# Performance work log

Measured on AMD Instinct MI355X. Metric: run time of the kernel, lower is better.

The kernel has to match this reference:

```python
import jax, jax.numpy as jnp
import numpy as np

TOP_K = 2


def setup_inputs() -> dict:
    key = jax.random.key(0)
    k1, k2, k3, k4 = jax.random.split(key, 4)
    B, S, H, I, E = 8, 2048, 768, 3072, 8
    x = jax.random.normal(k1, (B, S, H), dtype=jnp.float32)
    # kaiming_uniform-ish scale for weights
    router_w = jax.random.uniform(k2, (E, H), dtype=jnp.float32, minval=-1.0, maxval=1.0) * (1.0 / np.sqrt(H))
    up_w = jax.random.uniform(k3, (E, H, I), dtype=jnp.float32, minval=-1.0, maxval=1.0) * (1.0 / np.sqrt(H))
    down_w = jax.random.uniform(k4, (E, I, H), dtype=jnp.float32, minval=-1.0, maxval=1.0) * (1.0 / np.sqrt(I))
    return {"x": x, "router_w": router_w, "up_w": up_w, "down_w": down_w}


def reference(x, router_w, up_w, down_w):
    B, S, H = x.shape
    E = up_w.shape[0]
    T = B * S
    xf = x.reshape(T, H)
    # router: Linear(H -> E, bias=False) then softmax, top-k, renormalize
    logits = xf @ router_w.T                      # [T, E]
    probs = jax.nn.softmax(logits, axis=-1)
    top_w, top_i = jax.lax.top_k(probs, TOP_K)    # [T, K]
    top_w = top_w / jnp.sum(top_w, axis=-1, keepdims=True)
    # dense per-(token, expert) gate: zero for unselected experts
    gate = jnp.zeros((T, E), dtype=xf.dtype).at[jnp.arange(T)[:, None], top_i].add(top_w)
    # combine: sum_e gate[:, e] * down_e(gelu(up_e(x)))
    out = jnp.zeros_like(xf)
    for e in range(E):  # fixed small expert count; loop is structural, not over data dims
        h = jax.nn.gelu(xf @ up_w[e], approximate=False)   # exact GELU == torch F.gelu
        out = out + gate[:, e:e + 1] * (h @ down_w[e])
    return out.reshape(B, S, H)
```

## Files before the change

kernel.cpp:

```cpp
#include <hip/hip_runtime.h>

typedef short bf16x8 __attribute__((ext_vector_type(8)));
typedef float f32x4  __attribute__((ext_vector_type(4)));

#define T_TOK 16384
#define HD 768
#define ID 3072
#define NE 8
#define NT1MAX 136

__device__ __forceinline__ unsigned short f2bf(float f) {
    unsigned int u = __float_as_uint(f);
    unsigned int r = (u + 0x7FFFu + ((u >> 16) & 1u)) >> 16;
    return (unsigned short)r;
}

__device__ __forceinline__ void gload16(const void* g, void* l) {
    __builtin_amdgcn_global_load_lds(
        (const __attribute__((address_space(1))) void*)g,
        (__attribute__((address_space(3))) void*)l, 16, 0, 0);
}

__device__ __forceinline__ float gelu_f(float x) {
    float z = fabsf(x) * 0.70710678118f;
    float t = 1.0f / fmaf(0.3275911f, z, 1.0f);
    float p = t * fmaf(t, fmaf(t, fmaf(t, fmaf(t, 1.061405429f, -1.453152027f),
                                       1.421413741f), -0.284496736f), 0.254829592f);
    float e = 1.0f - p * __expf(-z * z);
    float erfv = (x >= 0.f) ? e : -e;
    return 0.5f * x * (1.0f + erfv);
}

__device__ __forceinline__ int xcd_swz(int bid, int nwg) {
    int q = nwg >> 3, rr = nwg & 7;
    int xcd = bid & 7, seq = bid >> 3;
    return (xcd < rr ? xcd * (q + 1) : rr * (q + 1) + (xcd - rr) * q) + seq;
}

__global__ __launch_bounds__(256) void k_tp(const float* __restrict__ in,
                                            unsigned short* __restrict__ out,
                                            int R, int C) {
    __shared__ float t[64][65];
    const float* ine = in + (size_t)blockIdx.z * R * C;
    unsigned short* oute = out + (size_t)blockIdx.z * R * C;
    int c0 = blockIdx.x * 64, r0 = blockIdx.y * 64;
    int lc = threadIdx.x & 63, lr4 = threadIdx.x >> 6;
#pragma unroll
    for (int i = 0; i < 16; i++) {
        int r = i * 4 + lr4;
        t[r][lc] = ine[(size_t)(r0 + r) * C + c0 + lc];
    }
    __syncthreads();
#pragma unroll
    for (int i = 0; i < 16; i++) {
        int r = i * 4 + lr4;
        oute[(size_t)(c0 + r) * R + r0 + lc] = f2bf(t[lc][r]);
    }
}

__global__ __launch_bounds__(256) void k_router(const float* __restrict__ x,
                                                const float* __restrict__ rw,
                                                unsigned short* __restrict__ xb,
                                                int* __restrict__ topE,
                                                float* __restrict__ topW) {
    __shared__ float lrw[NE * HD];
    for (int i = threadIdx.x; i < NE * HD; i += 256) lrw[i] = rw[i];
    {
        const float4* xs4 = (const float4*)(x + (size_t)blockIdx.x * 4 * HD);
        ushort4* xb4 = (ushort4*)(xb + (size_t)blockIdx.x * 4 * HD);
#pragma unroll
        for (int i = 0; i < 3; i++) {
            float4 v = xs4[threadIdx.x + i * 256];
            ushort4 o;
            o.x = f2bf(v.x); o.y = f2bf(v.y); o.z = f2bf(v.z); o.w = f2bf(v.w);
            xb4[threadIdx.x + i * 256] = o;
        }
    }
    __syncthreads();
    int lane = threadIdx.x & 63;
    int t = blockIdx.x * 4 + (threadIdx.x >> 6);
    const float* xr = x + (size_t)t * HD;
    float acc[NE] = {0, 0, 0, 0, 0, 0, 0, 0};
    for (int h = lane; h < HD; h += 64) {
        float xv = xr[h];
#pragma unroll
        for (int e = 0; e < NE; e++) acc[e] = fmaf(xv, lrw[e * HD + h], acc[e]);
    }
#pragma unroll
    for (int e = 0; e < NE; e++) {
        float v = acc[e];
#pragma unroll
        for (int o = 32; o > 0; o >>= 1) v += __shfl_xor(v, o, 64);
        acc[e] = v;
    }
    if (lane == 0) {
        int e1 = 0; float l1 = acc[0];
#pragma unroll
        for (int e = 1; e < NE; e++) if (acc[e] > l1) { l1 = acc[e]; e1 = e; }
        int e2 = -1; float l2 = -1e30f;
#pragma unroll
        for (int e = 0; e < NE; e++) if (e != e1 && acc[e] > l2) { l2 = acc[e]; e2 = e; }
        float ex = expf(l2 - l1);
        float w1 = 1.0f / (1.0f + ex);
        topE[2 * t] = e1; topE[2 * t + 1] = e2;
        topW[2 * t] = w1; topW[2 * t + 1] = ex * w1;
    }
}

__global__ __launch_bounds__(256) void k_scatter(const int* __restrict__ topE,
                                                 const float* __restrict__ topW,
                                                 int* __restrict__ counts,
                                                 int* __restrict__ tokL,
                                                 float* __restrict__ gateL) {
    __shared__ int lc[NE], lbase[NE];
    if (threadIdx.x < NE) lc[threadIdx.x] = 0;
    __syncthreads();
    int t = blockIdx.x * 256 + threadIdx.x;
    int e1 = topE[2 * t], e2 = topE[2 * t + 1];
    int p1 = atomicAdd(&lc[e1], 1);
    int p2 = atomicAdd(&lc[e2], 1);
    __syncthreads();
    if (threadIdx.x < NE) lbase[threadIdx.x] = atomicAdd(&counts[threadIdx.x], lc[threadIdx.x]);
    __syncthreads();
    int q1 = lbase[e1] + p1, q2 = lbase[e2] + p2;
    tokL[e1 * T_TOK + q1] = t;  gateL[e1 * T_TOK + q1] = topW[2 * t];
    tokL[e2 * T_TOK + q2] = t;  gateL[e2 * T_TOK + q2] = topW[2 * t + 1];
}

__global__ void k_desc(const int* __restrict__ counts, int* __restrict__ tileE,
                       int* __restrict__ tileM0) {
    if (threadIdx.x == 0 && blockIdx.x == 0) {
        int tl = 0;
        for (int e = 0; e < NE; e++) {
            int c = counts[e];
            int nt = (c + 255) >> 8;
            for (int t = 0; t < nt; t++) { tileE[tl] = e; tileM0[tl] = t << 8; tl++; }
        }
        for (; tl < NT1MAX; tl++) { tileE[tl] = -1; tileM0[tl] = 0; }
    }
}

__global__ __launch_bounds__(512, 1) void k_gemm1(
    const unsigned short* __restrict__ xb,
    const unsigned short* __restrict__ upt,
    const int* __restrict__ tokL,
    const int* __restrict__ counts,
    const int* __restrict__ tileE,
    const int* __restrict__ tileM0,
    unsigned short* __restrict__ h,
    int seg, int ntn, int ldh) {
    __shared__ __align__(16) char lds[5][32768];
    constexpr int NK = HD / 32;
    int L = xcd_swz(blockIdx.x, gridDim.x);
    int mt = L / ntn, ntl = L - mt * ntn;
    int e = tileE[mt];
    if (e < 0) return;
    int m0 = tileM0[mt];
    int nrow = min(256, counts[e] - m0);
    const int* tok = tokL + e * T_TOK + m0;
    int n0 = (seg * ntn + ntl) * 256;

    const int tid = threadIdx.x, lane = tid & 63, wid = tid >> 6;
    const int wm = wid >> 2, wn = wid & 3;
    const int g = lane >> 4, r = lane & 15;

    int ar0 = wid * 16 + r;
    int ar1 = 128 + wid * 16 + r;
    const char* a0 = (const char*)(xb + (size_t)tok[ar0 < nrow ? ar0 : 0] * HD) + g * 16;
    const char* a1 = (const char*)(xb + (size_t)tok[ar1 < nrow ? ar1 : 0] * HD) + g * 16;
    const char* bsl = (const char*)(upt + (size_t)e * ID * HD);
    const char* b0 = bsl + (size_t)(n0 + wid * 16 + r) * (HD * 2) + g * 16;
    const char* b1 = bsl + (size_t)(n0 + 128 + wid * 16 + r) * (HD * 2) + g * 16;
    const int dst = wid * 1024;

    auto issue = [&](int step, int slot) {
        char* base = &lds[slot][0];
        int kb = step * 64;
        gload16(a0 + kb, base + dst);
        gload16(a1 + kb, base + 8192 + dst);
        gload16(b0 + kb, base + 16384 + dst);
        gload16(b1 + kb, base + 24576 + dst);
    };

    f32x4 acc[8][4];
#pragma unroll
    for (int m = 0; m < 8; m++)
#pragma unroll
        for (int n = 0; n < 4; n++) acc[m][n] = (f32x4){0.f, 0.f, 0.f, 0.f};

    issue(0, 0); issue(1, 1); issue(2, 2); issue(3, 3);
    asm volatile("s_waitcnt vmcnt(12)" ::: "memory");
    __builtin_amdgcn_s_barrier();
    asm volatile("" ::: "memory");

    const int aoff = wm * 8192 + g * 256 + r * 16;
    const int boff = 16384 + wn * 4096 + g * 256 + r * 16;

    for (int k = 0; k < NK; k++) {
        char* base = &lds[k % 5][0];
        bf16x8 a[4], b[4];
#pragma unroll
        for (int n = 0; n < 4; n++) b[n] = *(const bf16x8*)(base + boff + n * 1024);
#pragma unroll
        for (int m = 0; m < 4; m++) a[m] = *(const bf16x8*)(base + aoff + m * 1024);
        issue(min(k + 4, NK - 1), (k + 4) % 5);
        __builtin_amdgcn_s_setprio(1);
#pragma unroll
        for (int m = 0; m < 4; m++)
#pragma unroll
            for (int n = 0; n < 4; n++)
                acc[m][n] = __builtin_amdgcn_mfma_f32_16x16x32_bf16(a[m], b[n], acc[m][n], 0, 0, 0);
        __builtin_amdgcn_s_setprio(0);
#pragma unroll
        for (int m = 0; m < 4; m++) a[m] = *(const bf16x8*)(base + aoff + (4 + m) * 1024);
        __builtin_amdgcn_s_setprio(1);
#pragma unroll
        for (int m = 0; m < 4; m++)
#pragma unroll
            for (int n = 0; n < 4; n++)
                acc[4 + m][n] = __builtin_amdgcn_mfma_f32_16x16x32_bf16(a[m], b[n], acc[4 + m][n], 0, 0, 0);
        __builtin_amdgcn_s_setprio(0);
        asm volatile("s_waitcnt vmcnt(12)" ::: "memory");
        __builtin_amdgcn_s_barrier();
        asm volatile("" ::: "memory");
    }
    asm volatile("s_waitcnt vmcnt(0)" ::: "memory");

#pragma unroll
    for (int m = 0; m < 8; m++)
#pragma unroll
        for (int j = 0; j < 4; j++) {
            int rl = wm * 128 + m * 16 + g * 4 + j;
            if (rl < nrow) {
                unsigned short* hr = h + (size_t)(mt * 256 + rl) * ldh + ntl * 256 + wn * 64 + r;
#pragma unroll
                for (int n = 0; n < 4; n++) hr[n * 16] = f2bf(gelu_f(acc[m][n][j]));
            }
        }
}

__global__ __launch_bounds__(512, 1) void k_gemm2(
    const unsigned short* __restrict__ h,
    const unsigned short* __restrict__ dnt,
    const int* __restrict__ tokL,
    const float* __restrict__ gateL,
    const int* __restrict__ counts,
    const int* __restrict__ tileE,
    const int* __restrict__ tileM0,
    float* __restrict__ out,
    int seg, int ldh, int nk) {
    __shared__ __align__(16) char lds[5][32768];
    int L = xcd_swz(blockIdx.x, gridDim.x);
    int mt = L / 3, ntl = L - mt * 3;
    int e = tileE[mt];
    if (e < 0) return;
    int m0 = tileM0[mt];
    int nrow = min(256, counts[e] - m0);
    const int* tok = tokL + e * T_TOK + m0;
    const float* gat = gateL + e * T_TOK + m0;
    int n0 = ntl * 256;

    const int tid = threadIdx.x, lane = tid & 63, wid = tid >> 6;
    const int wm = wid >> 2, wn = wid & 3;
    const int g = lane >> 4, r = lane & 15;

    int ar0 = wid * 16 + r;
    int ar1 = 128 + wid * 16 + r;
    const char* a0 = (const char*)h + ((size_t)(mt * 256 + ar0) * ldh) * 2 + g * 16;
    const char* a1 = (const char*)h + ((size_t)(mt * 256 + ar1) * ldh) * 2 + g * 16;
    const char* bsl = (const char*)(dnt + (size_t)e * ID * HD) + (size_t)seg * ldh * 2;
    const char* b0 = bsl + (size_t)(n0 + wid * 16 + r) * (ID * 2) + g * 16;
    const char* b1 = bsl + (size_t)(n0 + 128 + wid * 16 + r) * (ID * 2) + g * 16;
    const int dst = wid * 1024;

    auto issue = [&](int step, int slot) {
        char* base = &lds[slot][0];
        int kb = step * 64;
        gload16(a0 + kb, base + dst);
        gload16(a1 + kb, base + 8192 + dst);
        gload16(b0 + kb, base + 16384 + dst);
        gload16(b1 + kb, base + 24576 + dst);
    };

    f32x4 acc[8][4];
#pragma unroll
    for (int m = 0; m < 8; m++)
#pragma unroll
        for (int n = 0; n < 4; n++) acc[m][n] = (f32x4){0.f, 0.f, 0.f, 0.f};

    issue(0, 0); issue(1, 1); issue(2, 2); issue(3, 3);
    asm volatile("s_waitcnt vmcnt(12)" ::: "memory");
    __builtin_amdgcn_s_barrier();
    asm volatile("" ::: "memory");

    const int aoff = wm * 8192 + g * 256 + r * 16;
    const int boff = 16384 + wn * 4096 + g * 256 + r * 16;

    for (int k = 0; k < nk; k++) {
        char* base = &lds[k % 5][0];
        bf16x8 a[4], b[4];
#pragma unroll
        for (int n = 0; n < 4; n++) b[n] = *(const bf16x8*)(base + boff + n * 1024);
#pragma unroll
        for (int m = 0; m < 4; m++) a[m] = *(const bf16x8*)(base + aoff + m * 1024);
        issue(min(k + 4, nk - 1), (k + 4) % 5);
        __builtin_amdgcn_s_setprio(1);
#pragma unroll
        for (int m = 0; m < 4; m++)
#pragma unroll
            for (int n = 0; n < 4; n++)
                acc[m][n] = __builtin_amdgcn_mfma_f32_16x16x32_bf16(a[m], b[n], acc[m][n], 0, 0, 0);
        __builtin_amdgcn_s_setprio(0);
#pragma unroll
        for (int m = 0; m < 4; m++) a[m] = *(const bf16x8*)(base + aoff + (4 + m) * 1024);
        __builtin_amdgcn_s_setprio(1);
#pragma unroll
        for (int m = 0; m < 4; m++)
#pragma unroll
            for (int n = 0; n < 4; n++)
                acc[4 + m][n] = __builtin_amdgcn_mfma_f32_16x16x32_bf16(a[m], b[n], acc[4 + m][n], 0, 0, 0);
        __builtin_amdgcn_s_setprio(0);
        asm volatile("s_waitcnt vmcnt(12)" ::: "memory");
        __builtin_amdgcn_s_barrier();
        asm volatile("" ::: "memory");
    }
    asm volatile("s_waitcnt vmcnt(0)" ::: "memory");

#pragma unroll
    for (int m = 0; m < 8; m++)
#pragma unroll
        for (int j = 0; j < 4; j++) {
            int rl = wm * 128 + m * 16 + g * 4 + j;
            if (rl < nrow) {
                int t = tok[rl];
                float gv = gat[rl];
                float* orow = out + (size_t)t * HD + n0 + wn * 64 + r;
#pragma unroll
                for (int n = 0; n < 4; n++)
                    atomicAdd(orow + n * 16, gv * acc[m][n][j]);
            }
        }
}

__global__ __launch_bounds__(512, 2) void k_moe(
    const unsigned short* __restrict__ xb,
    const unsigned short* __restrict__ upt,
    const unsigned short* __restrict__ dnt,
    const int* __restrict__ counts,
    const int* __restrict__ tokL,
    const float* __restrict__ gateL,
    float* __restrict__ out) {
    __shared__ __align__(16) char lds[155648];
    char* xs = lds;
    char* hs = lds + 98304;
    char* ring = lds + 106496;

    const int e = blockIdx.x & 7;
    const int slot = blockIdx.x >> 3;
    const int cnt = counts[e];
    if (slot * 64 >= cnt) return;
    const int nrow = min(64, cnt - slot * 64);
    const int* tok = tokL + e * T_TOK + slot * 64;
    const float* gat = gateL + e * T_TOK + slot * 64;

    const int tid = threadIdx.x;
    const int lane = tid & 63;
    const int wid = tid >> 6;
    const int mi = wid >> 2, ni = wid & 3;

    const char* upe = (const char*)(upt + (size_t)e * ID * HD);
    const char* dne = (const char*)(dnt + (size_t)e * HD * ID);

    {
        int off = tid * 16;
#pragma unroll
        for (int s = 0; s < 12; s++) {
            int o = off + s * 8192;
            int m = o / 1536;
            int cb = o - m * 1536;
            int tk = (m < nrow) ? tok[m] : tok[0];
            const char* src = (const char*)xb + (size_t)tk * 1536 + (size_t)(cb ^ ((m & 7) << 4));
            gload16(src, xs + s * 8192 + wid * 1024);
        }
    }
    asm volatile("s_waitcnt vmcnt(0)" ::: "memory");
    __builtin_amdgcn_s_barrier();
    asm volatile("" ::: "memory");

    auto issue = [&](int s) {
        char* dstp = ring + (s % 6) * 8192 + wid * 1024;
        int ci = s / 24;
        int ph = s - ci * 24;
        int row = tid >> 3;
        int cb = (tid & 7) << 4;
        int scb = cb ^ ((row & 7) << 4);
        const char* src;
        if (ci >= 48) src = upe;
        else if (ph < 12) src = upe + (size_t)(ci * 64 + row) * 1536 + ph * 128 + scb;
        else              src = dne + (size_t)((ph - 12) * 64 + row) * 6144 + ci * 128 + scb;
        gload16(src, dstp);
    };

    f32x4 acc[2][12];
#pragma unroll
    for (int a = 0; a < 2; a++)
#pragma unroll
        for (int b = 0; b < 12; b++) acc[a][b] = (f32x4){0.f, 0.f, 0.f, 0.f};

    issue(0); issue(1); issue(2); issue(3);

    f32x4 acch[2];
    bf16x8 ha[2][2];

    for (int ci = 0; ci < 48; ci++) {
#pragma unroll
        for (int ks = 0; ks < 12; ks++) {
            issue(ci * 24 + ks + 4);
            asm volatile("s_waitcnt vmcnt(4)" ::: "memory");
            __builtin_amdgcn_s_barrier();
            asm volatile("" ::: "memory");
            char* buf = ring + (ks % 6) * 8192;
            if (ks == 0) { acch[0] = (f32x4){0.f,0.f,0.f,0.f}; acch[1] = (f32x4){0.f,0.f,0.f,0.f}; }
#pragma unroll
            for (int kkr = 0; kkr < 2; kkr++) {
                int bn = ni * 16 + (lane & 15);
                int bo = ((kkr * 32 + (lane >> 4) * 8) * 2) ^ ((bn & 7) << 4);
                bf16x8 bfrag = *(const bf16x8*)(buf + bn * 128 + bo);
#pragma unroll
                for (int mr = 0; mr < 2; mr++) {
                    int ar = mi * 32 + mr * 16 + (lane & 15);
                    int ao = ((ks * 64 + kkr * 32 + (lane >> 4) * 8) * 2) ^ ((ar & 7) << 4);
                    bf16x8 afrag = *(const bf16x8*)(xs + ar * 1536 + ao);
                    acch[mr] = __builtin_amdgcn_mfma_f32_16x16x32_bf16(afrag, bfrag, acch[mr], 0, 0, 0);
                }
            }
            if (ks == 11) {
#pragma unroll
                for (int mr = 0; mr < 2; mr++) {
                    int col = ni * 16 + (lane & 15);
#pragma unroll
                    for (int rr = 0; rr < 4; rr++) {
                        int m = mi * 32 + mr * 16 + (lane >> 4) * 4 + rr;
                        float v = acch[mr][rr];
                        *(unsigned short*)(hs + m * 128 + ((col * 2) ^ ((m & 7) << 4))) = f2bf(gelu_f(v));
                    }
                }
                asm volatile("s_waitcnt lgkmcnt(0)" ::: "memory");
            }
        }
#pragma unroll
        for (int j = 0; j < 12; j++) {
            issue(ci * 24 + 12 + j + 4);
            asm volatile("s_waitcnt vmcnt(4)" ::: "memory");
            __builtin_amdgcn_s_barrier();
            asm volatile("" ::: "memory");
            char* buf = ring + ((12 + j) % 6) * 8192;
            if (j == 0) {
#pragma unroll
                for (int mr = 0; mr < 2; mr++)
#pragma unroll
                    for (int kkr = 0; kkr < 2; kkr++) {
                        int ar = mi * 32 + mr * 16 + (lane & 15);
                        int ao = ((kkr * 32 + (lane >> 4) * 8) * 2) ^ ((ar & 7) << 4);
                        ha[mr][kkr] = *(const bf16x8*)(hs + ar * 128 + ao);
                    }
            }
#pragma unroll
            for (int kkr = 0; kkr < 2; kkr++) {
                int bn = ni * 16 + (lane & 15);
                int bo = ((kkr * 32 + (lane >> 4) * 8) * 2) ^ ((bn & 7) << 4);
                bf16x8 bfrag = *(const bf16x8*)(buf + bn * 128 + bo);
#pragma unroll
                for (int mr = 0; mr < 2; mr++)
                    acc[mr][j] = __builtin_amdgcn_mfma_f32_16x16x32_bf16(ha[mr][kkr], bfrag, acc[mr][j], 0, 0, 0);
            }
        }
    }

    int   t4[2][4];
    float g4[2][4];
#pragma unroll
    for (int mr = 0; mr < 2; mr++)
#pragma unroll
        for (int rr = 0; rr < 4; rr++) {
            int m = mi * 32 + mr * 16 + (lane >> 4) * 4 + rr;
            bool valid = m < nrow;
            t4[mr][rr] = valid ? tok[m] : -1;
            g4[mr][rr] = valid ? gat[m] : 0.f;
        }
#pragma unroll
    for (int mr = 0; mr < 2; mr++)
#pragma unroll
        for (int j = 0; j < 12; j++) {
            int colg = j * 64 + ni * 16 + (lane & 15);
#pragma unroll
            for (int rr = 0; rr < 4; rr++) {
                if (t4[mr][rr] >= 0)
                    atomicAdd(out + (size_t)t4[mr][rr] * HD + colg, g4[mr][rr] * acc[mr][j][rr]);
            }
        }
}

extern "C" void kernel_launch(void* const* d_in, const int* in_sizes, int n_in,
                              void* d_out, int out_size, void* d_ws, size_t ws_size,
                              hipStream_t stream) {
    const float* x  = (const float*)d_in[0];
    const float* rw = (const float*)d_in[1];
    const float* uw = (const float*)d_in[2];
    const float* dw = (const float*)d_in[3];
    float* out = (float*)d_out;

    size_t off = 0;
    char* base = (char*)d_ws;
    auto alloc = [&](size_t bytes) -> char* {
        char* p = base + off;
        off += (bytes + 1023) & ~(size_t)1023;
        return p;
    };
    unsigned short* xb   = (unsigned short*)alloc((size_t)T_TOK * HD * 2);
    unsigned short* upt  = (unsigned short*)alloc((size_t)NE * ID * HD * 2);
    unsigned short* dnt  = (unsigned short*)alloc((size_t)NE * HD * ID * 2);
    int*   topE   = (int*)alloc((size_t)T_TOK * 2 * 4);
    float* topW   = (float*)alloc((size_t)T_TOK * 2 * 4);
    int*   counts = (int*)alloc(256);
    int*   tileE  = (int*)alloc(NT1MAX * 4);
    int*   tileM0 = (int*)alloc(NT1MAX * 4);
    int*   tokL   = (int*)alloc((size_t)NE * T_TOK * 4);
    float* gateL  = (float*)alloc((size_t)NE * T_TOK * 4);
    size_t fixed = off;

    const int cand[6] = {1, 2, 3, 4, 6, 12};
    int S = 0;
    size_t hrows = (size_t)NT1MAX * 256;
    for (int i = 0; i < 6; i++) {
        size_t hb = hrows * (ID / cand[i]) * 2;
        if (fixed + hb <= ws_size) { S = cand[i]; break; }
    }
    unsigned short* h = (unsigned short*)(base + fixed);

    hipMemsetAsync(d_out, 0, (size_t)T_TOK * HD * 4, stream);
    hipMemsetAsync(counts, 0, 256, stream);

    k_tp<<<dim3(ID / 64, HD / 64, NE), 256, 0, stream>>>(uw, upt, HD, ID);
    k_tp<<<dim3(HD / 64, ID / 64, NE), 256, 0, stream>>>(dw, dnt, ID, HD);
    k_router<<<T_TOK / 4, 256, 0, stream>>>(x, rw, xb, topE, topW);
    k_scatter<<<T_TOK / 256, 256, 0, stream>>>(topE, topW, counts, tokL, gateL);

    if (S > 0) {
        int ldh = ID / S;
        int ntn = ldh / 256;
        int nk2 = ldh / 32;
        k_desc<<<1, 64, 0, stream>>>(counts, tileE, tileM0);
        for (int sg = 0; sg < S; sg++) {
            k_gemm1<<<NT1MAX * ntn, 512, 0, stream>>>(xb, upt, tokL, counts, tileE, tileM0,
                                                      h, sg, ntn, ldh);
            k_gemm2<<<NT1MAX * 3, 512, 0, stream>>>(h, dnt, tokL, gateL, counts, tileE, tileM0,
                                                    out, sg, ldh, nk2);
        }
    } else {
        k_moe<<<2048, 512, 0, stream>>>(xb, upt, dnt, counts, tokL, gateL, out);
    }
}
```

Before: 754.9 us.

## Pre-pack weights, gathered activations and hidden tiles into MFMA-ready contiguous blocks

Replaces the transposes with packing kernels that write up/down weights as contiguous 16 KB tiles already in the LDS fragment order. A new gather kernel packs the routed token rows of x into per-tile bf16 blocks, so the router no longer converts x. GEMM1 writes h in the same packed layout, so both GEMMs stream their operands with fully contiguous global-to-LDS loads instead of strided row gathers. This adds an extra gather pass and scattered 2-byte stores in the GEMM1 epilogue. It also drops the fused k_moe fallback and always uses the segmented path.

Result: faster. 698.5 us (-7.5%).

```diff
diff --git a/kernel.cpp b/kernel.cpp
--- a/kernel.cpp
+++ b/kernel.cpp
@@ -37,45 +37,52 @@
     return (xcd < rr ? xcd * (q + 1) : rr * (q + 1) + (xcd - rr) * q) + seq;
 }
 
-__global__ __launch_bounds__(256) void k_tp(const float* __restrict__ in,
-                                            unsigned short* __restrict__ out,
-                                            int R, int C) {
-    __shared__ float t[64][65];
-    const float* ine = in + (size_t)blockIdx.z * R * C;
-    unsigned short* oute = out + (size_t)blockIdx.z * R * C;
-    int c0 = blockIdx.x * 64, r0 = blockIdx.y * 64;
-    int lc = threadIdx.x & 63, lr4 = threadIdx.x >> 6;
-#pragma unroll
-    for (int i = 0; i < 16; i++) {
-        int r = i * 4 + lr4;
-        t[r][lc] = ine[(size_t)(r0 + r) * C + c0 + lc];
-    }
-    __syncthreads();
-#pragma unroll
-    for (int i = 0; i < 16; i++) {
-        int r = i * 4 + lr4;
-        oute[(size_t)(c0 + r) * R + r0 + lc] = f2bf(t[lc][r]);
+__global__ __launch_bounds__(256) void k_wpack_up(const float* __restrict__ uw,
+                                                  unsigned short* __restrict__ upk) {
+    int blk = blockIdx.x;
+    int ks = blk % 24, rem = blk / 24;
+    int it = rem % 12, e = rem / 12;
+    const float* src = uw + (size_t)e * HD * ID;
+    char* dst = (char*)upk + (size_t)blk * 16384;
+#pragma unroll
+    for (int i4 = 0; i4 < 4; i4++) {
+        int u = threadIdx.x + i4 * 256;
+        int c = u >> 6, g = (u >> 4) & 3, r = u & 15;
+        int icol = it * 256 + c * 16 + r;
+        int h0 = ks * 32 + g * 8;
+        unsigned short o[8];
+#pragma unroll
+        for (int b = 0; b < 8; b++) o[b] = f2bf(src[(size_t)(h0 + b) * ID + icol]);
+        *(uint4*)(dst + (size_t)u * 16) = *(const uint4*)o;
+    }
+}
+
+__global__ __launch_bounds__(256) void k_wpack_dn(const float* __restrict__ dw,
+                                                  unsigned short* __restrict__ dnk) {
+    int blk = blockIdx.x;
+    int ks = blk % 96, rem = blk / 96;
+    int nt = rem % 3, e = rem / 3;
+    const float* src = dw + (size_t)e * ID * HD;
+    char* dst = (char*)dnk + (size_t)blk * 16384;
+#pragma unroll
+    for (int i4 = 0; i4 < 4; i4++) {
+        int u = threadIdx.x + i4 * 256;
+        int c = u >> 6, g = (u >> 4) & 3, r = u & 15;
+        int hcol = nt * 256 + c * 16 + r;
+        int i0 = ks * 32 + g * 8;
+        unsigned short o[8];
+#pragma unroll
+        for (int b = 0; b < 8; b++) o[b] = f2bf(src[(size_t)(i0 + b) * HD + hcol]);
+        *(uint4*)(dst + (size_t)u * 16) = *(const uint4*)o;
     }
 }
 
 __global__ __launch_bounds__(256) void k_router(const float* __restrict__ x,
                                                 const float* __restrict__ rw,
-                                                unsigned short* __restrict__ xb,
                                                 int* __restrict__ topE,
                                                 float* __restrict__ topW) {
     __shared__ float lrw[NE * HD];
     for (int i = threadIdx.x; i < NE * HD; i += 256) lrw[i] = rw[i];
-    {
-        const float4* xs4 = (const float4*)(x + (size_t)blockIdx.x * 4 * HD);
-        ushort4* xb4 = (ushort4*)(xb + (size_t)blockIdx.x * 4 * HD);
-#pragma unroll
-        for (int i = 0; i < 3; i++) {
-            float4 v = xs4[threadIdx.x + i * 256];
-            ushort4 o;
-            o.x = f2bf(v.x); o.y = f2bf(v.y); o.z = f2bf(v.z); o.w = f2bf(v.w);
-            xb4[threadIdx.x + i * 256] = o;
-        }
-    }
     __syncthreads();
     int lane = threadIdx.x & 63;
     int t = blockIdx.x * 4 + (threadIdx.x >> 6);
@@ -140,15 +147,42 @@
     }
 }
 
+__global__ __launch_bounds__(256) void k_gpack(const float* __restrict__ x,
+                                               const int* __restrict__ tokL,
+                                               const int* __restrict__ counts,
+                                               const int* __restrict__ tileE,
+                                               const int* __restrict__ tileM0,
+                                               unsigned short* __restrict__ xgk) {
+    int blk = blockIdx.x;
+    int mt = blk / 24, ks = blk % 24;
+    int e = tileE[mt];
+    if (e < 0) return;
+    int m0 = tileM0[mt];
+    int nrow = min(256, counts[e] - m0);
+    const int* tok = tokL + e * T_TOK + m0;
+    char* dst = (char*)xgk + (size_t)blk * 16384;
+#pragma unroll
+    for (int i4 = 0; i4 < 4; i4++) {
+        int u = threadIdx.x + i4 * 256;
+        int c = u >> 6, g = (u >> 4) & 3, r = u & 15;
+        int row = c * 16 + r;
+        int tk = tok[row < nrow ? row : 0];
+        const float* s = x + (size_t)tk * HD + ks * 32 + g * 8;
+        unsigned short o[8];
+#pragma unroll
+        for (int b = 0; b < 8; b++) o[b] = f2bf(s[b]);
+        *(uint4*)(dst + (size_t)u * 16) = *(const uint4*)o;
+    }
+}
+
 __global__ __launch_bounds__(512, 1) void k_gemm1(
-    const unsigned short* __restrict__ xb,
-    const unsigned short* __restrict__ upt,
-    const int* __restrict__ tokL,
+    const unsigned short* __restrict__ xgk,
+    const unsigned short* __restrict__ upk,
     const int* __restrict__ counts,
     const int* __restrict__ tileE,
     const int* __restrict__ tileM0,
-    unsigned short* __restrict__ h,
-    int seg, int ntn, int ldh) {
+    unsigned short* __restrict__ hk,
+    int seg, int ntn, int nk2) {
     __shared__ __align__(16) char lds[5][32768];
     constexpr int NK = HD / 32;
     int L = xcd_swz(blockIdx.x, gridDim.x);
@@ -157,29 +191,25 @@
     if (e < 0) return;
     int m0 = tileM0[mt];
     int nrow = min(256, counts[e] - m0);
-    const int* tok = tokL + e * T_TOK + m0;
-    int n0 = (seg * ntn + ntl) * 256;
 
     const int tid = threadIdx.x, lane = tid & 63, wid = tid >> 6;
     const int wm = wid >> 2, wn = wid & 3;
     const int g = lane >> 4, r = lane & 15;
 
-    int ar0 = wid * 16 + r;
-    int ar1 = 128 + wid * 16 + r;
-    const char* a0 = (const char*)(xb + (size_t)tok[ar0 < nrow ? ar0 : 0] * HD) + g * 16;
-    const char* a1 = (const char*)(xb + (size_t)tok[ar1 < nrow ? ar1 : 0] * HD) + g * 16;
-    const char* bsl = (const char*)(upt + (size_t)e * ID * HD);
-    const char* b0 = bsl + (size_t)(n0 + wid * 16 + r) * (HD * 2) + g * 16;
-    const char* b1 = bsl + (size_t)(n0 + 128 + wid * 16 + r) * (HD * 2) + g * 16;
-    const int dst = wid * 1024;
+    const char* abase = (const char*)xgk + (size_t)mt * (24 * 16384)
+                        + (size_t)(2 * wid) * 1024 + (size_t)lane * 16;
+    const char* bbase = (const char*)upk + (size_t)((e * 12 + seg * ntn + ntl) * 24) * 16384
+                        + (size_t)(2 * wid) * 1024 + (size_t)lane * 16;
+    const int dstoff = 2 * wid * 1024;
 
     auto issue = [&](int step, int slot) {
         char* base = &lds[slot][0];
-        int kb = step * 64;
-        gload16(a0 + kb, base + dst);
-        gload16(a1 + kb, base + 8192 + dst);
-        gload16(b0 + kb, base + 16384 + dst);
-        gload16(b1 + kb, base + 24576 + dst);
+        const char* as = abase + (size_t)step * 16384;
+        const char* bs = bbase + (size_t)step * 16384;
+        gload16(as,        base + dstoff);
+        gload16(as + 1024, base + dstoff + 1024);
+        gload16(bs,        base + 16384 + dstoff);
+        gload16(bs + 1024, base + 16384 + dstoff + 1024);
     };
 
     f32x4 acc[8][4];
@@ -226,29 +256,35 @@
     }
     asm volatile("s_waitcnt vmcnt(0)" ::: "memory");
 
+    char* hbase = (char*)hk + (size_t)mt * ((size_t)nk2 * 16384);
 #pragma unroll
     for (int m = 0; m < 8; m++)
 #pragma unroll
         for (int j = 0; j < 4; j++) {
             int rl = wm * 128 + m * 16 + g * 4 + j;
             if (rl < nrow) {
-                unsigned short* hr = h + (size_t)(mt * 256 + rl) * ldh + ntl * 256 + wn * 64 + r;
-#pragma unroll
-                for (int n = 0; n < 4; n++) hr[n * 16] = f2bf(gelu_f(acc[m][n][j]));
+                int c = rl >> 4, rr = rl & 15;
+#pragma unroll
+                for (int n = 0; n < 4; n++) {
+                    int col = ntl * 256 + wn * 64 + n * 16 + r;
+                    int ksl = col >> 5, gg = (col >> 3) & 3, b = col & 7;
+                    *(unsigned short*)(hbase + (size_t)ksl * 16384 + c * 1024 + gg * 256 + rr * 16 + b * 2)
+                        = f2bf(gelu_f(acc[m][n][j]));
+                }
             }
         }
 }
 
 __global__ __launch_bounds__(512, 1) void k_gemm2(
-    const unsigned short* __restrict__ h,
-    const unsigned short* __restrict__ dnt,
+    const unsigned short* __restrict__ hk,
+    const unsigned short* __restrict__ dnk,
     const int* __restrict__ tokL,
     const float* __restrict__ gateL,
     const int* __restrict__ counts,
     const int* __restrict__ tileE,
     const int* __restrict__ tileM0,
     float* __restrict__ out,
-    int seg, int ldh, int nk) {
+    int seg, int nk2) {
     __shared__ __align__(16) char lds[5][32768];
     int L = xcd_swz(blockIdx.x, gridDim.x);
     int mt = L / 3, ntl = L - mt * 3;
@@ -264,22 +300,20 @@
     const int wm = wid >> 2, wn = wid & 3;
     const int g = lane >> 4, r = lane & 15;
 
-    int ar0 = wid * 16 + r;
-    int ar1 = 128 + wid * 16 + r;
-    const char* a0 = (const char*)h + ((size_t)(mt * 256 + ar0) * ldh) * 2 + g * 16;
-    const char* a1 = (const char*)h + ((size_t)(mt * 256 + ar1) * ldh) * 2 + g * 16;
-    const char* bsl = (const char*)(dnt + (size_t)e * ID * HD) + (size_t)seg * ldh * 2;
-    const char* b0 = bsl + (size_t)(n0 + wid * 16 + r) * (ID * 2) + g * 16;
-    const char* b1 = bsl + (size_t)(n0 + 128 + wid * 16 + r) * (ID * 2) + g * 16;
-    const int dst = wid * 1024;
+    const char* abase = (const char*)hk + (size_t)mt * ((size_t)nk2 * 16384)
+                        + (size_t)(2 * wid) * 1024 + (size_t)lane * 16;
+    const char* bbase = (const char*)dnk + (size_t)((e * 3 + ntl) * 96 + seg * nk2) * 16384
+                        + (size_t)(2 * wid) * 1024 + (size_t)lane * 16;
+    const int dstoff = 2 * wid * 1024;
 
     auto issue = [&](int step, int slot) {
         char* base = &lds[slot][0];
-        int kb = step * 64;
-        gload16(a0 + kb, base + dst);
-        gload16(a1 + kb, base + 8192 + dst);
-        gload16(b0 + kb, base + 16384 + dst);
-        gload16(b1 + kb, base + 24576 + dst);
+        const char* as = abase + (size_t)step * 16384;
+        const char* bs = bbase + (size_t)step * 16384;
+        gload16(as,        base + dstoff);
+        gload16(as + 1024, base + dstoff + 1024);
+        gload16(bs,        base + 16384 + dstoff);
+        gload16(bs + 1024, base + 16384 + dstoff + 1024);
     };
 
     f32x4 acc[8][4];
@@ -296,14 +330,14 @@
     const int aoff = wm * 8192 + g * 256 + r * 16;
     const int boff = 16384 + wn * 4096 + g * 256 + r * 16;
 
-    for (int k = 0; k < nk; k++) {
+    for (int k = 0; k < nk2; k++) {
         char* base = &lds[k % 5][0];
         bf16x8 a[4], b[4];
 #pragma unroll
         for (int n = 0; n < 4; n++) b[n] = *(const bf16x8*)(base + boff + n * 1024);
 #pragma unroll
         for (int m = 0; m < 4; m++) a[m] = *(const bf16x8*)(base + aoff + m * 1024);
-        issue(min(k + 4, nk - 1), (k + 4) % 5);
+        issue(min(k + 4, nk2 - 1), (k + 4) % 5);
         __builtin_amdgcn_s_setprio(1);
 #pragma unroll
         for (int m = 0; m < 4; m++)
@@ -338,165 +372,6 @@
 #pragma unroll
                 for (int n = 0; n < 4; n++)
                     atomicAdd(orow + n * 16, gv * acc[m][n][j]);
-            }
-        }
-}
-
-__global__ __launch_bounds__(512, 2) void k_moe(
-    const unsigned short* __restrict__ xb,
-    const unsigned short* __restrict__ upt,
-    const unsigned short* __restrict__ dnt,
-    const int* __restrict__ counts,
-    const int* __restrict__ tokL,
-    const float* __restrict__ gateL,
-    float* __restrict__ out) {
-    __shared__ __align__(16) char lds[155648];
-    char* xs = lds;
-    char* hs = lds + 98304;
-    char* ring = lds + 106496;
-
-    const int e = blockIdx.x & 7;
-    const int slot = blockIdx.x >> 3;
-    const int cnt = counts[e];
-    if (slot * 64 >= cnt) return;
-    const int nrow = min(64, cnt - slot * 64);
-    const int* tok = tokL + e * T_TOK + slot * 64;
-    const float* gat = gateL + e * T_TOK + slot * 64;
-
-    const int tid = threadIdx.x;
-    const int lane = tid & 63;
-    const int wid = tid >> 6;
-    const int mi = wid >> 2, ni = wid & 3;
-
-    const char* upe = (const char*)(upt + (size_t)e * ID * HD);
-    const char* dne = (const char*)(dnt + (size_t)e * HD * ID);
-
-    {
-        int off = tid * 16;
-#pragma unroll
-        for (int s = 0; s < 12; s++) {
-            int o = off + s * 8192;
-            int m = o / 1536;
-            int cb = o - m * 1536;
-            int tk = (m < nrow) ? tok[m] : tok[0];
-            const char* src = (const char*)xb + (size_t)tk * 1536 + (size_t)(cb ^ ((m & 7) << 4));
-            gload16(src, xs + s * 8192 + wid * 1024);
-        }
-    }
-    asm volatile("s_waitcnt vmcnt(0)" ::: "memory");
-    __builtin_amdgcn_s_barrier();
-    asm volatile("" ::: "memory");
-
-    auto issue = [&](int s) {
-        char* dstp = ring + (s % 6) * 8192 + wid * 1024;
-        int ci = s / 24;
-        int ph = s - ci * 24;
-        int row = tid >> 3;
-        int cb = (tid & 7) << 4;
-        int scb = cb ^ ((row & 7) << 4);
-        const char* src;
-        if (ci >= 48) src = upe;
-        else if (ph < 12) src = upe + (size_t)(ci * 64 + row) * 1536 + ph * 128 + scb;
-        else              src = dne + (size_t)((ph - 12) * 64 + row) * 6144 + ci * 128 + scb;
-        gload16(src, dstp);
-    };
-
-    f32x4 acc[2][12];
-#pragma unroll
-    for (int a = 0; a < 2; a++)
-#pragma unroll
-        for (int b = 0; b < 12; b++) acc[a][b] = (f32x4){0.f, 0.f, 0.f, 0.f};
-
-    issue(0); issue(1); issue(2); issue(3);
-
-    f32x4 acch[2];
-    bf16x8 ha[2][2];
-
-    for (int ci = 0; ci < 48; ci++) {
-#pragma unroll
-        for (int ks = 0; ks < 12; ks++) {
-            issue(ci * 24 + ks + 4);
-            asm volatile("s_waitcnt vmcnt(4)" ::: "memory");
-            __builtin_amdgcn_s_barrier();
-            asm volatile("" ::: "memory");
-            char* buf = ring + (ks % 6) * 8192;
-            if (ks == 0) { acch[0] = (f32x4){0.f,0.f,0.f,0.f}; acch[1] = (f32x4){0.f,0.f,0.f,0.f}; }
-#pragma unroll
-            for (int kkr = 0; kkr < 2; kkr++) {
-                int bn = ni * 16 + (lane & 15);
-                int bo = ((kkr * 32 + (lane >> 4) * 8) * 2) ^ ((bn & 7) << 4);
-                bf16x8 bfrag = *(const bf16x8*)(buf + bn * 128 + bo);
-#pragma unroll
-                for (int mr = 0; mr < 2; mr++) {
-                    int ar = mi * 32 + mr * 16 + (lane & 15);
-                    int ao = ((ks * 64 + kkr * 32 + (lane >> 4) * 8) * 2) ^ ((ar & 7) << 4);
-                    bf16x8 afrag = *(const bf16x8*)(xs + ar * 1536 + ao);
-                    acch[mr] = __builtin_amdgcn_mfma_f32_16x16x32_bf16(afrag, bfrag, acch[mr], 0, 0, 0);
-                }
-            }
-            if (ks == 11) {
-#pragma unroll
-                for (int mr = 0; mr < 2; mr++) {
-                    int col = ni * 16 + (lane & 15);
-#pragma unroll
-                    for (int rr = 0; rr < 4; rr++) {
-                        int m = mi * 32 + mr * 16 + (lane >> 4) * 4 + rr;
-                        float v = acch[mr][rr];
-                        *(unsigned short*)(hs + m * 128 + ((col * 2) ^ ((m & 7) << 4))) = f2bf(gelu_f(v));
-                    }
-                }
-                asm volatile("s_waitcnt lgkmcnt(0)" ::: "memory");
-            }
-        }
-#pragma unroll
-        for (int j = 0; j < 12; j++) {
-            issue(ci * 24 + 12 + j + 4);
-            asm volatile("s_waitcnt vmcnt(4)" ::: "memory");
-            __builtin_amdgcn_s_barrier();
-            asm volatile("" ::: "memory");
-            char* buf = ring + ((12 + j) % 6) * 8192;
-            if (j == 0) {
-#pragma unroll
-                for (int mr = 0; mr < 2; mr++)
-#pragma unroll
-                    for (int kkr = 0; kkr < 2; kkr++) {
-                        int ar = mi * 32 + mr * 16 + (lane & 15);
-                        int ao = ((kkr * 32 + (lane >> 4) * 8) * 2) ^ ((ar & 7) << 4);
-                        ha[mr][kkr] = *(const bf16x8*)(hs + ar * 128 + ao);
-                    }
-            }
-#pragma unroll
-            for (int kkr = 0; kkr < 2; kkr++) {
-                int bn = ni * 16 + (lane & 15);
-                int bo = ((kkr * 32 + (lane >> 4) * 8) * 2) ^ ((bn & 7) << 4);
-                bf16x8 bfrag = *(const bf16x8*)(buf + bn * 128 + bo);
-#pragma unroll
-                for (int mr = 0; mr < 2; mr++)
-                    acc[mr][j] = __builtin_amdgcn_mfma_f32_16x16x32_bf16(ha[mr][kkr], bfrag, acc[mr][j], 0, 0, 0);
-            }
-        }
-    }
-
-    int   t4[2][4];
-    float g4[2][4];
-#pragma unroll
-    for (int mr = 0; mr < 2; mr++)
-#pragma unroll
-        for (int rr = 0; rr < 4; rr++) {
-            int m = mi * 32 + mr * 16 + (lane >> 4) * 4 + rr;
-            bool valid = m < nrow;
-            t4[mr][rr] = valid ? tok[m] : -1;
-            g4[mr][rr] = valid ? gat[m] : 0.f;
-        }
-#pragma unroll
-    for (int mr = 0; mr < 2; mr++)
-#pragma unroll
-        for (int j = 0; j < 12; j++) {
-            int colg = j * 64 + ni * 16 + (lane & 15);
-#pragma unroll
-            for (int rr = 0; rr < 4; rr++) {
-                if (t4[mr][rr] >= 0)
-                    atomicAdd(out + (size_t)t4[mr][rr] * HD + colg, g4[mr][rr] * acc[mr][j][rr]);
             }
         }
 }
@@ -517,9 +392,8 @@
         off += (bytes + 1023) & ~(size_t)1023;
         return p;
     };
-    unsigned short* xb   = (unsigned short*)alloc((size_t)T_TOK * HD * 2);
-    unsigned short* upt  = (unsigned short*)alloc((size_t)NE * ID * HD * 2);
-    unsigned short* dnt  = (unsigned short*)alloc((size_t)NE * HD * ID * 2);
+    unsigned short* upk  = (unsigned short*)alloc((size_t)NE * ID * HD * 2);
+    unsigned short* dnk  = (unsigned short*)alloc((size_t)NE * ID * HD * 2);
     int*   topE   = (int*)alloc((size_t)T_TOK * 2 * 4);
     float* topW   = (float*)alloc((size_t)T_TOK * 2 * 4);
     int*   counts = (int*)alloc(256);
@@ -527,37 +401,34 @@
     int*   tileM0 = (int*)alloc(NT1MAX * 4);
     int*   tokL   = (int*)alloc((size_t)NE * T_TOK * 4);
     float* gateL  = (float*)alloc((size_t)NE * T_TOK * 4);
+    unsigned short* xgk = (unsigned short*)alloc((size_t)NT1MAX * 24 * 16384);
     size_t fixed = off;
 
     const int cand[6] = {1, 2, 3, 4, 6, 12};
-    int S = 0;
-    size_t hrows = (size_t)NT1MAX * 256;
+    int S = 12;
     for (int i = 0; i < 6; i++) {
-        size_t hb = hrows * (ID / cand[i]) * 2;
+        size_t hb = (size_t)NT1MAX * 256 * (ID / cand[i]) * 2;
         if (fixed + hb <= ws_size) { S = cand[i]; break; }
     }
-    unsigned short* h = (unsigned short*)(base + fixed);
+    unsigned short* hk = (unsigned short*)(base + fixed);
 
     hipMemsetAsync(d_out, 0, (size_t)T_TOK * HD * 4, stream);
     hipMemsetAsync(counts, 0, 256, stream);
 
-    k_tp<<<dim3(ID / 64, HD / 64, NE), 256, 0, stream>>>(uw, upt, HD, ID);
-    k_tp<<<dim3(HD / 64, ID / 64, NE), 256, 0, stream>>>(dw, dnt, ID, HD);
-    k_router<<<T_TOK / 4, 256, 0, stream>>>(x, rw, xb, topE, topW);
+    k_wpack_up<<<NE * 12 * 24, 256, 0, stream>>>(uw, upk);
+    k_wpack_dn<<<NE * 3 * 96, 256, 0, stream>>>(dw, dnk);
+    k_router<<<T_TOK / 4, 256, 0, stream>>>(x, rw, topE, topW);
     k_scatter<<<T_TOK / 256, 256, 0, stream>>>(topE, topW, counts, tokL, gateL);
-
-    if (S > 0) {
-        int ldh = ID / S;
-        int ntn = ldh / 256;
-        int nk2 = ldh / 32;
-        k_desc<<<1, 64, 0, stream>>>(counts, tileE, tileM0);
-        for (int sg = 0; sg < S; sg++) {
-            k_gemm1<<<NT1MAX * ntn, 512, 0, stream>>>(xb, upt, tokL, counts, tileE, tileM0,
-                                                      h, sg, ntn, ldh);
-            k_gemm2<<<NT1MAX * 3, 512, 0, stream>>>(h, dnt, tokL, gateL, counts, tileE, tileM0,
-                                                    out, sg, ldh, nk2);
-        }
-    } else {
-        k_moe<<<2048, 512, 0, stream>>>(xb, upt, dnt, counts, tokL, gateL, out);
-    }
-}
+    k_desc<<<1, 64, 0, stream>>>(counts, tileE, tileM0);
+    k_gpack<<<NT1MAX * 24, 256, 0, stream>>>(x, tokL, counts, tileE, tileM0, xgk);
+
+    int ldh = ID / S;
+    int ntn = ldh / 256;
+    int nk2 = ldh / 32;
+    for (int sg = 0; sg < S; sg++) {
+        k_gemm1<<<NT1MAX * ntn, 512, 0, stream>>>(xgk, upk, counts, tileE, tileM0,
+                                                  hk, sg, ntn, nk2);
+        k_gemm2<<<NT1MAX * 3, 512, 0, stream>>>(hk, dnk, tokL, gateL, counts, tileE, tileM0,
+                                                out, sg, nk2);
+    }
+}
```
